# Performance work log

Hardware: AMD Instinct MI355X
Metric: run time of the kernel (lower is better)

The kernel has to match this reference:

```python
import jax, jax.numpy as jnp
import numpy as np

NUM_PATCHES = 16
FILTER_SIZE = 4
IN_CHANNELS = 64
OUT_CHANNELS = 256
BATCH = 64


def setup_inputs() -> dict:
    key = jax.random.key(0)
    k1, k2 = jax.random.split(key)
    D = NUM_PATCHES * FILTER_SIZE
    x = jax.random.normal(k1, (BATCH, IN_CHANNELS, D, D), dtype=jnp.float32)
    w = jax.random.normal(
        k2,
        (OUT_CHANNELS, IN_CHANNELS, NUM_PATCHES, NUM_PATCHES, FILTER_SIZE ** 2),
        dtype=jnp.float32,
    )
    return {"x": x, "w": w}


def reference(x, w):
    # x: (N, C, D, D) with D = P*f ; w: (O, C, P, P, f^2)
    N, C, D, _ = x.shape
    O, _, P, _, f2 = w.shape
    f = int(round(f2 ** 0.5))
    # non-overlapping unfold: (N,C,P,f,P,f) -> (N,C,P,P,f,f) -> (N,C,P,P,f^2)
    patches = x.reshape(N, C, P, f, P, f).transpose(0, 1, 2, 4, 3, 5).reshape(N, C, P, P, f2)
    # locally-connected contraction over in_channels and filter elements
    y = jnp.einsum('ncpqf,ocpqf->nopq', patches, w)
    scale = 1.0 / jnp.sqrt(jnp.asarray(f2 * C, dtype=x.dtype))
    return jax.nn.relu(y * scale)
```

## Files before the change

### kernel.cpp

```cpp
#include <hip/hip_runtime.h>


typedef short bf16x8 __attribute__((ext_vector_type(8)));
typedef short bf16x4 __attribute__((ext_vector_type(4)));
typedef float f32x4  __attribute__((ext_vector_type(4)));

__device__ __forceinline__ short f2bf(float f) {
    union { float f; unsigned u; } v; v.f = f;
    return (short)((v.u + 0x7FFFu + ((v.u >> 16) & 1u)) >> 16);
}

__device__ __forceinline__ bf16x8 pack8(f32x4 a, f32x4 b) {
    bf16x8 r;
    r[0] = f2bf(a[0]); r[1] = f2bf(a[1]); r[2] = f2bf(a[2]); r[3] = f2bf(a[3]);
    r[4] = f2bf(b[0]); r[5] = f2bf(b[1]); r[6] = f2bf(b[2]); r[7] = f2bf(b[3]);
    return r;
}

__global__ __launch_bounds__(256)
void prep_unfold(const float* __restrict__ x, short* __restrict__ xT) {
    __shared__ __align__(16) char tile[16 * 2056];
    const int bid = blockIdx.x;
    const int p = bid >> 6, c = bid & 63;
    const int t = (int)threadIdx.x;

#pragma unroll
    for (int it = 0; it < 16; ++it) {
        const int id = it * 256 + t;
        const int n = id >> 6, fr = (id >> 4) & 3, cq = id & 15;
        const f32x4 v = *(const f32x4*)(x + (size_t)n * 262144u
                                          + (size_t)c * 4096u
                                          + (size_t)(4 * p + fr) * 64u
                                          + (size_t)(cq * 4));
        bf16x4 b; b[0] = f2bf(v[0]); b[1] = f2bf(v[1]);
                  b[2] = f2bf(v[2]); b[3] = f2bf(v[3]);
        *(bf16x4*)(tile + cq * 2056 + (fr >> 1) * 1024 + n * 16
                        + (fr & 1) * 8) = b;
    }
    __syncthreads();

#pragma unroll
    for (int it = 0; it < 8; ++it) {
        const int id = it * 256 + t;
        const int q = id >> 7, s = id & 127;
        const int koct = s >> 6, n = s & 63;
        const bf16x8 v = *(const bf16x8*)(tile + q * 2056 + koct * 1024 + n * 16);
        *(bf16x8*)(xT + (size_t)(p * 16 + q) * 65536u + (size_t)c * 1024u
                      + (size_t)koct * 512u + (size_t)n * 8u) = v;
    }
}

__global__ __launch_bounds__(512)
void locblock_gemm(const short* __restrict__ xT, const float* __restrict__ w,
                   float* __restrict__ ws2) {
    __shared__ __align__(16) char smem[2][32768];

    const int hw = blockIdx.x;
    const int lb = (hw & 7) * 32 + (hw >> 3);
    const int p  = lb >> 4;
    const int q2 = (lb >> 1) & 7;
    const int oh = lb & 1;

    const int tid  = (int)threadIdx.x;
    const int lane = tid & 63;
    const int wv   = tid >> 6;
    const int l15  = lane & 15;
    const int kq   = lane >> 4;
    const int qw   = wv & 1;
    const int nc   = wv >> 1;

    const short* asrc = xT + (size_t)(p * 16 + q2 * 2 + qw) * 65536u
                           + (size_t)(kq >> 1) * 1024u + (size_t)(kq & 1) * 512u
                           + (size_t)l15 * 8u;

    const float* bsrc[4];
#pragma unroll
    for (int j = 0; j < 4; ++j) {
        const int id = j * 512 + tid;
        const int ol = id >> 4, u = id & 15;
        bsrc[j] = w + (size_t)(oh * 128 + ol) * 262144u + (size_t)(u >> 3) * 4096u
                    + (size_t)p * 256u + (size_t)(q2 * 32) + (size_t)((u & 7) * 4);
    }
    int wofs[4];
#pragma unroll
    for (int j = 0; j < 4; ++j) {
        const int id = j * 512 + tid;
        const int ol = id >> 4;
        wofs[j] = ol * 64 + (((tid & 15) ^ (ol & 15)) * 4);
    }
    const int u1 = (kq >> 1) * 8 + qw * 4 + (kq & 1) * 2;
    int boff[2][2];
#pragma unroll
    for (int nf = 0; nf < 2; ++nf) {
        const int ol = nc * 32 + nf * 16 + l15;
        boff[nf][0] = ol * 256 + (((u1)     ^ l15) * 16);
        boff[nf][1] = ol * 256 + (((u1 + 1) ^ l15) * 16);
    }

    f32x4 acc[4][2];
#pragma unroll
    for (int mf = 0; mf < 4; ++mf)
#pragma unroll
        for (int nf = 0; nf < 2; ++nf)
            acc[mf][nf] = (f32x4){0.f, 0.f, 0.f, 0.f};

    bf16x8 as0[4], as1[4];
    f32x4  bs0[4], bs1[4];

#define ISSUE_A(AS, T)                                                        \
    _Pragma("unroll") for (int mf = 0; mf < 4; ++mf)                          \
        AS[mf] = *(const bf16x8*)(asrc + (size_t)(T) * 2048u + mf * 128);
#define ISSUE_B(BS, T)                                                        \
    _Pragma("unroll") for (int j = 0; j < 4; ++j)                             \
        BS[j] = *(const f32x4*)(bsrc[j] + (size_t)(T) * 8192u);
#define DSWRITE(BS, BUF)                                                      \
    { float* Wb = (float*)(smem[BUF]);                                        \
      _Pragma("unroll") for (int j = 0; j < 4; ++j)                           \
          *(f32x4*)(Wb + wofs[j]) = BS[j]; }
#define COMPUTE(AS, BUF)                                                      \
    { const char* Lb = smem[BUF];                                             \
      bf16x8 bv0 = pack8(*(const f32x4*)(Lb + boff[0][0]),                    \
                         *(const f32x4*)(Lb + boff[0][1]));                   \
      bf16x8 bv1 = pack8(*(const f32x4*)(Lb + boff[1][0]),                    \
                         *(const f32x4*)(Lb + boff[1][1]));                   \
      _Pragma("unroll") for (int mf = 0; mf < 4; ++mf) {                      \
          acc[mf][0] = __builtin_amdgcn_mfma_f32_16x16x32_bf16(               \
              AS[mf], bv0, acc[mf][0], 0, 0, 0);                              \
          acc[mf][1] = __builtin_amdgcn_mfma_f32_16x16x32_bf16(               \
              AS[mf], bv1, acc[mf][1], 0, 0, 0);                              \
      } }

    ISSUE_A(as0, 0); ISSUE_A(as1, 1);
    ISSUE_B(bs0, 0); ISSUE_B(bs1, 1);
    asm volatile("s_waitcnt vmcnt(0)" ::: "memory");
    DSWRITE(bs0, 0);
    asm volatile("s_waitcnt lgkmcnt(0)" ::: "memory");
    __builtin_amdgcn_s_barrier();

#pragma unroll 1
    for (int t = 0; t < 30; t += 2) {
        COMPUTE(as0, 0);
        ISSUE_A(as0, t + 2);
        ISSUE_B(bs0, t + 2);
        asm volatile("s_waitcnt vmcnt(8)" ::: "memory");
        DSWRITE(bs1, 1);
        asm volatile("s_waitcnt lgkmcnt(0)" ::: "memory");
        __builtin_amdgcn_s_barrier();
        COMPUTE(as1, 1);
        ISSUE_A(as1, t + 3);
        ISSUE_B(bs1, t + 3);
        asm volatile("s_waitcnt vmcnt(8)" ::: "memory");
        DSWRITE(bs0, 0);
        asm volatile("s_waitcnt lgkmcnt(0)" ::: "memory");
        __builtin_amdgcn_s_barrier();
    }
    COMPUTE(as0, 0);
    asm volatile("s_waitcnt vmcnt(0)" ::: "memory");
    DSWRITE(bs1, 1);
    asm volatile("s_waitcnt lgkmcnt(0)" ::: "memory");
    __builtin_amdgcn_s_barrier();
    COMPUTE(as1, 1);

#undef ISSUE_A
#undef ISSUE_B
#undef DSWRITE
#undef COMPUTE

    const float scale = 0.03125f;
    const int pq = p * 16 + q2 * 2 + qw;
#pragma unroll
    for (int mf = 0; mf < 4; ++mf)
#pragma unroll
        for (int nf = 0; nf < 2; ++nf) {
            const int o  = oh * 128 + nc * 32 + nf * 16 + l15;
            const int n0 = mf * 16 + kq * 4;
            f32x4 r;
#pragma unroll
            for (int j = 0; j < 4; ++j)
                r[j] = fmaxf(acc[mf][nf][j] * scale, 0.0f);
            *(f32x4*)(ws2 + (size_t)pq * 16384u + (size_t)o * 64u + n0) = r;
        }
}

__global__ __launch_bounds__(256)
void finish_transpose(const float* __restrict__ ws2, float* __restrict__ out) {
    __shared__ float tile[256 * 68];
    const int o = blockIdx.x;
    const int t = (int)threadIdx.x;

#pragma unroll
    for (int it = 0; it < 16; ++it) {
        const int chunk = it * 256 + t;
        const int pq = chunk >> 4, ng = chunk & 15;
        const f32x4 v = *(const f32x4*)(ws2 + (size_t)pq * 16384u
                                            + (size_t)o * 64u + ng * 4);
        *(f32x4*)&tile[pq * 68 + ng * 4] = v;
    }
    __syncthreads();

    const int n = t >> 2, pqq = t & 3;
#pragma unroll
    for (int i = 0; i < 16; ++i) {
        const int pq0 = i * 16 + pqq * 4;
        f32x4 r;
#pragma unroll
        for (int k = 0; k < 4; ++k)
            r[k] = tile[(pq0 + k) * 68 + n];
        *(f32x4*)(out + (size_t)n * 65536u + (size_t)o * 256u + pq0) = r;
    }
}

extern "C" void kernel_launch(void* const* d_in, const int* in_sizes, int n_in,
                              void* d_out, int out_size, void* d_ws, size_t ws_size,
                              hipStream_t stream) {
    const float* x = (const float*)d_in[0];
    const float* w = (const float*)d_in[1];
    float* out = (float*)d_out;
    short* xT  = (short*)d_ws;
    float* ws2 = (float*)((char*)d_ws + (33554432));
    prep_unfold     <<<dim3(1024), dim3(256), 0, stream>>>(x, xT);
    locblock_gemm   <<<dim3(256),  dim3(512), 0, stream>>>(xT, w, ws2);
    finish_transpose<<<dim3(256),  dim3(256), 0, stream>>>(ws2, out);
}
```

Baseline: 104.4 us.

## Load weights straight into registers and write output directly, dropping transpose kernel

The GEMM kernel no longer stages the weight tile through shared memory with barriers. Each lane now loads its own weight fragments from global memory into registers and converts them to bf16 there. The epilogue writes relu-scaled results straight into the final output layout, so the separate transpose kernel and its workspace round-trip are removed. The trade-off is less coalesced weight loads (32-byte runs per lane) and scattered 4-byte output stores with a stride of 64K floats.

```diff
diff --git a/kernel.cpp b/kernel.cpp
--- a/kernel.cpp
+++ b/kernel.cpp
@@ -52,9 +52,7 @@
 
 __global__ __launch_bounds__(512)
 void locblock_gemm(const short* __restrict__ xT, const float* __restrict__ w,
-                   float* __restrict__ ws2) {
-    __shared__ __align__(16) char smem[2][32768];
-
+                   float* __restrict__ out) {
     const int hw = blockIdx.x;
     const int lb = (hw & 7) * 32 + (hw >> 3);
     const int p  = lb >> 4;
@@ -73,28 +71,14 @@
                            + (size_t)(kq >> 1) * 1024u + (size_t)(kq & 1) * 512u
                            + (size_t)l15 * 8u;
 
-    const float* bsrc[4];
-#pragma unroll
-    for (int j = 0; j < 4; ++j) {
-        const int id = j * 512 + tid;
-        const int ol = id >> 4, u = id & 15;
-        bsrc[j] = w + (size_t)(oh * 128 + ol) * 262144u + (size_t)(u >> 3) * 4096u
-                    + (size_t)p * 256u + (size_t)(q2 * 32) + (size_t)((u & 7) * 4);
-    }
-    int wofs[4];
-#pragma unroll
-    for (int j = 0; j < 4; ++j) {
-        const int id = j * 512 + tid;
-        const int ol = id >> 4;
-        wofs[j] = ol * 64 + (((tid & 15) ^ (ol & 15)) * 4);
-    }
     const int u1 = (kq >> 1) * 8 + qw * 4 + (kq & 1) * 2;
-    int boff[2][2];
+    const float* bsrc[2];
 #pragma unroll
     for (int nf = 0; nf < 2; ++nf) {
-        const int ol = nc * 32 + nf * 16 + l15;
-        boff[nf][0] = ol * 256 + (((u1)     ^ l15) * 16);
-        boff[nf][1] = ol * 256 + (((u1 + 1) ^ l15) * 16);
+        const int o = oh * 128 + nc * 32 + nf * 16 + l15;
+        bsrc[nf] = w + (size_t)o * 262144u + (size_t)(u1 >> 3) * 4096u
+                     + (size_t)p * 256u + (size_t)(q2 * 32)
+                     + (size_t)((u1 & 7) * 4);
     }
 
     f32x4 acc[4][2];
@@ -105,24 +89,19 @@
             acc[mf][nf] = (f32x4){0.f, 0.f, 0.f, 0.f};
 
     bf16x8 as0[4], as1[4];
-    f32x4  bs0[4], bs1[4];
+    f32x4  bs0[2][2], bs1[2][2];
 
-#define ISSUE_A(AS, T)                                                        \
+#define ISSUE(AS, BS, T)                                                      \
+    _Pragma("unroll") for (int nf = 0; nf < 2; ++nf) {                        \
+        BS[nf][0] = *(const f32x4*)(bsrc[nf] + (size_t)(T) * 8192u);          \
+        BS[nf][1] = *(const f32x4*)(bsrc[nf] + (size_t)(T) * 8192u + 4);      \
+    }                                                                         \
     _Pragma("unroll") for (int mf = 0; mf < 4; ++mf)                          \
         AS[mf] = *(const bf16x8*)(asrc + (size_t)(T) * 2048u + mf * 128);
-#define ISSUE_B(BS, T)                                                        \
-    _Pragma("unroll") for (int j = 0; j < 4; ++j)                             \
-        BS[j] = *(const f32x4*)(bsrc[j] + (size_t)(T) * 8192u);
-#define DSWRITE(BS, BUF)                                                      \
-    { float* Wb = (float*)(smem[BUF]);                                        \
-      _Pragma("unroll") for (int j = 0; j < 4; ++j)                           \
-          *(f32x4*)(Wb + wofs[j]) = BS[j]; }
-#define COMPUTE(AS, BUF)                                                      \
-    { const char* Lb = smem[BUF];                                             \
-      bf16x8 bv0 = pack8(*(const f32x4*)(Lb + boff[0][0]),                    \
-                         *(const f32x4*)(Lb + boff[0][1]));                   \
-      bf16x8 bv1 = pack8(*(const f32x4*)(Lb + boff[1][0]),                    \
-                         *(const f32x4*)(Lb + boff[1][1]));                   \
+
+#define COMPUTE(AS, BS)                                                       \
+    { bf16x8 bv0 = pack8(BS[0][0], BS[0][1]);                                 \
+      bf16x8 bv1 = pack8(BS[1][0], BS[1][1]);                                 \
       _Pragma("unroll") for (int mf = 0; mf < 4; ++mf) {                      \
           acc[mf][0] = __builtin_amdgcn_mfma_f32_16x16x32_bf16(               \
               AS[mf], bv0, acc[mf][0], 0, 0, 0);                              \
@@ -130,40 +109,27 @@
               AS[mf], bv1, acc[mf][1], 0, 0, 0);                              \
       } }
 
-    ISSUE_A(as0, 0); ISSUE_A(as1, 1);
-    ISSUE_B(bs0, 0); ISSUE_B(bs1, 1);
-    asm volatile("s_waitcnt vmcnt(0)" ::: "memory");
-    DSWRITE(bs0, 0);
-    asm volatile("s_waitcnt lgkmcnt(0)" ::: "memory");
-    __builtin_amdgcn_s_barrier();
-
+    ISSUE(as0, bs0, 0);
+    ISSUE(as1, bs1, 1);
 #pragma unroll 1
     for (int t = 0; t < 30; t += 2) {
-        COMPUTE(as0, 0);
-        ISSUE_A(as0, t + 2);
-        ISSUE_B(bs0, t + 2);
         asm volatile("s_waitcnt vmcnt(8)" ::: "memory");
-        DSWRITE(bs1, 1);
-        asm volatile("s_waitcnt lgkmcnt(0)" ::: "memory");
-        __builtin_amdgcn_s_barrier();
-        COMPUTE(as1, 1);
-        ISSUE_A(as1, t + 3);
-        ISSUE_B(bs1, t + 3);
+        __builtin_amdgcn_sched_barrier(0);
+        COMPUTE(as0, bs0);
+        ISSUE(as0, bs0, t + 2);
         asm volatile("s_waitcnt vmcnt(8)" ::: "memory");
-        DSWRITE(bs0, 0);
-        asm volatile("s_waitcnt lgkmcnt(0)" ::: "memory");
-        __builtin_amdgcn_s_barrier();
+        __builtin_amdgcn_sched_barrier(0);
+        COMPUTE(as1, bs1);
+        ISSUE(as1, bs1, t + 3);
     }
-    COMPUTE(as0, 0);
+    asm volatile("s_waitcnt vmcnt(8)" ::: "memory");
+    __builtin_amdgcn_sched_barrier(0);
+    COMPUTE(as0, bs0);
     asm volatile("s_waitcnt vmcnt(0)" ::: "memory");
-    DSWRITE(bs1, 1);
-    asm volatile("s_waitcnt lgkmcnt(0)" ::: "memory");
-    __builtin_amdgcn_s_barrier();
-    COMPUTE(as1, 1);
+    __builtin_amdgcn_sched_barrier(0);
+    COMPUTE(as1, bs1);
 
-#undef ISSUE_A
-#undef ISSUE_B
-#undef DSWRITE
+#undef ISSUE
 #undef COMPUTE
 
     const float scale = 0.03125f;
@@ -172,42 +138,13 @@
     for (int mf = 0; mf < 4; ++mf)
 #pragma unroll
         for (int nf = 0; nf < 2; ++nf) {
-            const int o  = oh * 128 + nc * 32 + nf * 16 + l15;
-            const int n0 = mf * 16 + kq * 4;
-            f32x4 r;
+            const int o = oh * 128 + nc * 32 + nf * 16 + l15;
+            float* ob = out + (size_t)(mf * 16 + kq * 4) * 65536u
+                            + (size_t)o * 256u + pq;
 #pragma unroll
             for (int j = 0; j < 4; ++j)
-                r[j] = fmaxf(acc[mf][nf][j] * scale, 0.0f);
-            *(f32x4*)(ws2 + (size_t)pq * 16384u + (size_t)o * 64u + n0) = r;
+                ob[(size_t)j * 65536u] = fmaxf(acc[mf][nf][j] * scale, 0.0f);
         }
-}
-
-__global__ __launch_bounds__(256)
-void finish_transpose(const float* __restrict__ ws2, float* __restrict__ out) {
-    __shared__ float tile[256 * 68];
-    const int o = blockIdx.x;
-    const int t = (int)threadIdx.x;
-
-#pragma unroll
-    for (int it = 0; it < 16; ++it) {
-        const int chunk = it * 256 + t;
-        const int pq = chunk >> 4, ng = chunk & 15;
-        const f32x4 v = *(const f32x4*)(ws2 + (size_t)pq * 16384u
-                                            + (size_t)o * 64u + ng * 4);
-        *(f32x4*)&tile[pq * 68 + ng * 4] = v;
-    }
-    __syncthreads();
-
-    const int n = t >> 2, pqq = t & 3;
-#pragma unroll
-    for (int i = 0; i < 16; ++i) {
-        const int pq0 = i * 16 + pqq * 4;
-        f32x4 r;
-#pragma unroll
-        for (int k = 0; k < 4; ++k)
-            r[k] = tile[(pq0 + k) * 68 + n];
-        *(f32x4*)(out + (size_t)n * 65536u + (size_t)o * 256u + pq0) = r;
-    }
 }
 
 extern "C" void kernel_launch(void* const* d_in, const int* in_sizes, int n_in,
@@ -217,8 +154,6 @@
     const float* w = (const float*)d_in[1];
     float* out = (float*)d_out;
     short* xT  = (short*)d_ws;
-    float* ws2 = (float*)((char*)d_ws + (33554432));
-    prep_unfold     <<<dim3(1024), dim3(256), 0, stream>>>(x, xT);
-    locblock_gemm   <<<dim3(256),  dim3(512), 0, stream>>>(xT, w, ws2);
-    finish_transpose<<<dim3(256),  dim3(256), 0, stream>>>(ws2, out);
+    prep_unfold  <<<dim3(1024), dim3(256), 0, stream>>>(x, xT);
+    locblock_gemm<<<dim3(256),  dim3(512), 0, stream>>>(xT, w, out);
 }
```

After: 135.2 us. +29.6%, slower.
